# Optimization experiments

Measured on AMD Instinct MI355X. Metric: run time of the kernel, lower is better.

## Reference

```python
import jax, jax.numpy as jnp
import numpy as np

D_MODEL = 768
N_HEAD = 12
D_FF = 2048
KEEP_RATIO = 0.6
EPS = 1e-6


def rmsnorm(x, g):
    var = jnp.mean(x * x, axis=-1, keepdims=True)
    return x * jax.lax.rsqrt(var + EPS) * g


def setup_inputs() -> dict:
    key = jax.random.key(0)
    ks = jax.random.split(key, 16)
    B, S, D, F = 2, 2048, D_MODEL, D_FF
    s = 0.02
    inp = {
        "hidden": jax.random.normal(ks[0], (B, S, D), jnp.float32),
        "attn_mask": jnp.tril(jnp.ones((S, S), dtype=bool)),
        "temperature": 1,
        "wq": jax.random.normal(ks[1], (D, D), jnp.float32) * s,
        "wk": jax.random.normal(ks[2], (D, D), jnp.float32) * s,
        "wv": jax.random.normal(ks[3], (D, D), jnp.float32) * s,
        "wo": jax.random.normal(ks[4], (D, D), jnp.float32) * s,
        "w1": jax.random.normal(ks[5], (D, F), jnp.float32) * s,
        "w3": jax.random.normal(ks[6], (D, F), jnp.float32) * s,
        "w2": jax.random.normal(ks[7], (F, D), jnp.float32) * s,
        "g1": jnp.ones((D,), jnp.float32),
        "g2": jnp.ones((D,), jnp.float32),
        "w_mod": jax.random.normal(ks[8], (D,), jnp.float32) * s,
        "b_mod": jnp.zeros((), jnp.float32),
        "w_tok": jax.random.normal(ks[9], (D,), jnp.float32) * s,
        "b_tok": jnp.zeros((), jnp.float32),
        "w_gate": jax.random.normal(ks[10], (D, D), jnp.float32) * s,
        "b_gate": jnp.zeros((D,), jnp.float32),
    }
    return inp


def reference(hidden, attn_mask, temperature, wq, wk, wv, wo, w1, w3, w2,
              g1, g2, w_mod, b_mod, w_tok, b_tok, w_gate, b_gate):
    B, S, D = hidden.shape
    H = N_HEAD
    Dh = D // H

    # depth router: sigmoid(linear / temperature)
    depth_logits = jnp.einsum("bsd,d->bs", hidden, w_mod) + b_mod
    depth_probs = jax.nn.sigmoid(depth_logits / temperature)
    active = (depth_probs > 0.5).astype(hidden.dtype)[..., None]  # [B,S,1]

    normed = rmsnorm(hidden, g1)

    # token router: sigmoid scores, hard top-k keep mask at base keep ratio
    token_scores = jax.nn.sigmoid(jnp.einsum("bsd,d->bs", normed, w_tok) + b_tok)
    k = max(1, int(S * KEEP_RATIO))
    kth = jax.lax.top_k(token_scores, k)[0][:, -1:]  # [B,1]
    token_mask = (token_scores >= kth).astype(hidden.dtype)  # [B,S]

    # multi-head attention over normed
    q = jnp.einsum("bsd,de->bse", normed, wq).reshape(B, S, H, Dh)
    kk = jnp.einsum("bsd,de->bse", normed, wk).reshape(B, S, H, Dh)
    v = jnp.einsum("bsd,de->bse", normed, wv).reshape(B, S, H, Dh)
    logits = jnp.einsum("bqhd,bkhd->bhqk", q, kk) / jnp.sqrt(jnp.float32(Dh))
    logits = jnp.where(attn_mask[None, None, :, :], logits, jnp.float32(-1e9))
    probs = jax.nn.softmax(logits, axis=-1)
    ctx = jnp.einsum("bhqk,bkhd->bqhd", probs, v).reshape(B, S, D)
    attn_out = jnp.einsum("bsd,de->bse", ctx, wo)

    attn_out = attn_out * token_mask[..., None]
    hidden = hidden + attn_out * active  # dropout = identity (eval)

    # ACM gate: x * sigmoid(Wx + b)
    n2 = rmsnorm(hidden, g2)
    gated = n2 * jax.nn.sigmoid(jnp.einsum("bsd,de->bse", n2, w_gate) + b_gate)

    # SwiGLU MLP
    mlp = jnp.einsum("bsf,fd->bsd",
                     jax.nn.silu(jnp.einsum("bsd,df->bsf", gated, w1))
                     * jnp.einsum("bsd,df->bsf", gated, w3), w2)
    hidden = hidden + mlp * active
    return hidden, depth_probs, token_mask
```

## Files before the change

### kernel.cpp

```cpp
#include <hip/hip_runtime.h>


typedef float f32x4 __attribute__((ext_vector_type(4)));
typedef __bf16 bf16x8 __attribute__((ext_vector_type(8)));
typedef unsigned int u32;

#define DEV static __device__ __forceinline__

constexpr int SEQ = 2048, DIM = 768, NH = 12;
constexpr int KKEEP = 1228;

DEV f32x4 mfma16(bf16x8 a, bf16x8 b, f32x4 c) {
  return __builtin_amdgcn_mfma_f32_16x16x32_bf16(a, b, c, 0, 0, 0);
}
DEV float sigm(float x) { return 1.0f / (1.0f + __expf(-x)); }
DEV bf16x8 ld8(const __bf16* p) { return *reinterpret_cast<const bf16x8*>(p); }
DEV void st8(__bf16* p, bf16x8 v) { *reinterpret_cast<bf16x8*>(p) = v; }
DEV int swzo(int row, int u) { return row * 64 + ((u ^ (row & 7)) << 3); }

template <int NZ>
struct PtrPack { const float* s[NZ]; };

template <int NZ>
__global__ void k_transpose_castz(PtrPack<NZ> pp, __bf16* __restrict__ dst0,
                                  int K, int N, size_t dstride) {
  const float* __restrict__ src = pp.s[blockIdx.z];
  __bf16* __restrict__ dst = dst0 + (size_t)blockIdx.z * dstride;
  __shared__ float tile[32][33];
  const int tx = threadIdx.x, ty = threadIdx.y;
  const int n0 = blockIdx.x * 32, k0 = blockIdx.y * 32;
  for (int i = 0; i < 4; ++i)
    tile[ty + 8 * i][tx] = src[(size_t)(k0 + ty + 8 * i) * N + n0 + tx];
  __syncthreads();
  for (int i = 0; i < 4; ++i)
    dst[(size_t)(n0 + ty + 8 * i) * K + k0 + tx] = (__bf16)tile[tx][ty + 8 * i];
}

__global__ void k_transpose_bf(const __bf16* __restrict__ src,
                               __bf16* __restrict__ dst) {
  __shared__ __bf16 t64[64][66];
  const int tx = threadIdx.x, ty = threadIdx.y;
  const int c0 = blockIdx.x * 64, r0 = blockIdx.y * 64;
#pragma unroll
  for (int i = 0; i < 8; ++i) {
    union { u32 uu; __bf16 hh[2]; } cv;
    cv.uu = *reinterpret_cast<const u32*>(src + (size_t)(r0 + ty + 8 * i) * 768 +
                                          c0 + tx * 2);
    t64[ty + 8 * i][tx * 2] = cv.hh[0];
    t64[ty + 8 * i][tx * 2 + 1] = cv.hh[1];
  }
  __syncthreads();
#pragma unroll
  for (int i = 0; i < 8; ++i) {
    union { u32 uu; __bf16 hh[2]; } cv;
    cv.hh[0] = t64[tx * 2][ty + 8 * i];
    cv.hh[1] = t64[tx * 2 + 1][ty + 8 * i];
    *reinterpret_cast<u32*>(dst + (size_t)(c0 + ty + 8 * i) * 4096 + r0 + tx * 2) =
        cv.uu;
  }
}

__global__ __launch_bounds__(256) void k_router(
    const float* __restrict__ hid, const float* __restrict__ g1,
    const float* __restrict__ wmod, const float* __restrict__ bmod,
    const float* __restrict__ wtok, const float* __restrict__ btok,
    const int* __restrict__ temp, __bf16* __restrict__ normed,
    float* __restrict__ depth_out, float* __restrict__ actF,
    float* __restrict__ tokL) {
  const int t = blockIdx.x, tid = threadIdx.x;
  const float* x = hid + (size_t)t * DIM;
  float xs[3], gs[3], ss = 0.f, dm = 0.f, dt = 0.f;
  for (int j = 0; j < 3; ++j) {
    const int i = tid + 256 * j;
    const float xv = x[i], g = g1[i];
    xs[j] = xv; gs[j] = g;
    ss += xv * xv;
    dm += xv * wmod[i];
    dt += xv * g * wtok[i];
  }
  for (int m = 32; m >= 1; m >>= 1) {
    ss += __shfl_xor(ss, m);
    dm += __shfl_xor(dm, m);
    dt += __shfl_xor(dt, m);
  }
  __shared__ float red[4][3];
  if ((tid & 63) == 0) { red[tid >> 6][0] = ss; red[tid >> 6][1] = dm; red[tid >> 6][2] = dt; }
  __syncthreads();
  ss = red[0][0] + red[1][0] + red[2][0] + red[3][0];
  dm = red[0][1] + red[1][1] + red[2][1] + red[3][1];
  dt = red[0][2] + red[1][2] + red[2][2] + red[3][2];
  const float rms = rsqrtf(ss / 768.0f + 1e-6f);
  if (tid == 0) {
    const int iv = temp[0];
    const float T = (iv > -100000 && iv < 100000) ? (float)iv : __int_as_float(iv);
    const float z = (dm + bmod[0]) / T;
    depth_out[t] = sigm(z);
    actF[t] = z > 0.0f ? 1.0f : 0.0f;
    tokL[t] = rms * dt + btok[0];
  }
  for (int j = 0; j < 3; ++j) {
    const int i = tid + 256 * j;
    normed[(size_t)t * DIM + i] = (__bf16)(xs[j] * rms * gs[j]);
  }
}

__global__ __launch_bounds__(256) void k_count(
    const float* __restrict__ tokL, float* __restrict__ kth_out) {
  const int b = blockIdx.y, tid = threadIdx.x;
  __shared__ float vals[2048];
  const float* L = tokL + (size_t)b * 2048;
#pragma unroll
  for (int j = 0; j < 8; ++j) vals[tid + 256 * j] = L[tid + 256 * j];
  __syncthreads();
  const int cand = blockIdx.x * 128 + (tid >> 1);
  const int half = tid & 1;
  const float e = vals[cand];
  int gt = 0, ge = 0;
  const float4* v4 = reinterpret_cast<const float4*>(vals) + half * 256;
#pragma unroll 8
  for (int j = 0; j < 256; ++j) {
    const float4 q = v4[j];
    gt += (q.x > e) + (q.y > e) + (q.z > e) + (q.w > e);
    ge += (q.x >= e) + (q.y >= e) + (q.z >= e) + (q.w >= e);
  }
  gt += __shfl_xor(gt, 1);
  ge += __shfl_xor(ge, 1);
  if (half == 0 && gt < KKEEP && KKEEP <= ge) kth_out[b] = e;
}

__global__ __launch_bounds__(256) void k_mask(
    const float* __restrict__ tokL, const float* __restrict__ kth,
    const float* __restrict__ actF, float* __restrict__ mask_out,
    float* __restrict__ maskact) {
  const int i = blockIdx.x * 256 + threadIdx.x;
  const int b = i >> 11;
  const float m = (tokL[i] >= kth[b]) ? 1.f : 0.f;
  mask_out[i] = m;
  maskact[i] = m * actF[i];
}

__global__ __launch_bounds__(256) void k_rmsnorm2(
    const float* __restrict__ h2, const float* __restrict__ g2,
    __bf16* __restrict__ n2) {
  const int t = blockIdx.x, tid = threadIdx.x;
  const float* x = h2 + (size_t)t * DIM;
  float xs[3], ss = 0.f;
  for (int j = 0; j < 3; ++j) { const float v = x[tid + 256 * j]; xs[j] = v; ss += v * v; }
  for (int m = 32; m >= 1; m >>= 1) ss += __shfl_xor(ss, m);
  __shared__ float red[4];
  if ((tid & 63) == 0) red[tid >> 6] = ss;
  __syncthreads();
  ss = red[0] + red[1] + red[2] + red[3];
  const float rms = rsqrtf(ss / 768.0f + 1e-6f);
  for (int j = 0; j < 3; ++j) {
    const int i = tid + 256 * j;
    n2[(size_t)t * DIM + i] = (__bf16)(xs[j] * rms * g2[i]);
  }
}

template <int EPI, int MI>
__global__ __launch_bounds__(256) void k_gemm(
    const __bf16* __restrict__ A, const __bf16* __restrict__ BT,
    int N, int K, size_t bt_stride, size_t out_stride,
    __bf16* __restrict__ outB, float* __restrict__ outF,
    const float* __restrict__ epF, const __bf16* __restrict__ epB,
    const float* __restrict__ rowsc, const float* __restrict__ bias) {
  constexpr int BM = MI * 32;
  __shared__ __align__(16) __bf16 As[BM * 64];
  __shared__ __align__(16) __bf16 Bs[128 * 64];
  const int tid = threadIdx.x;
  const int lane = tid & 63, w = tid >> 6;
  const int wr = w >> 1, wc = w & 1;
  const int f = lane & 15, e = lane >> 4;
  const int m0 = blockIdx.y * BM, n0 = blockIdx.x * 128;
  const __bf16* Bz = BT + (size_t)blockIdx.z * bt_stride;

  const int rowA = (MI == 4) ? (tid >> 1) : (tid >> 2);
  const int uA0  = (MI == 4) ? ((tid & 1) * 4) : ((tid & 3) * 2);
  const int rowB = tid >> 1, uB0 = (tid & 1) * 4;
  const __bf16* ApR = A + (size_t)(m0 + rowA) * K;
  const __bf16* BpR = Bz + (size_t)(n0 + rowB) * K;

  bf16x8 ya[MI], yb[4];
  auto LOADY = [&](int k0) {
#pragma unroll
    for (int j = 0; j < MI; ++j) ya[j] = ld8(ApR + k0 + (uA0 + j) * 8);
#pragma unroll
    for (int j = 0; j < 4; ++j) yb[j] = ld8(BpR + k0 + (uB0 + j) * 8);
  };
  auto STORE = [&]() {
#pragma unroll
    for (int j = 0; j < MI; ++j) st8(&As[swzo(rowA, uA0 + j)], ya[j]);
#pragma unroll
    for (int j = 0; j < 4; ++j) st8(&Bs[swzo(rowB, uB0 + j)], yb[j]);
  };

  f32x4 acc[MI][4] = {};
  LOADY(0);
  for (int k0 = 0; k0 < K; k0 += 64) {
    __syncthreads();
    STORE();
    if (k0 + 64 < K) LOADY(k0 + 64);
    __syncthreads();
    bf16x8 afl[MI], afh[MI], bfl[4], bfh[4];
#pragma unroll
    for (int mi = 0; mi < MI; ++mi) {
      const int row = wr * (MI * 16) + mi * 16 + f;
      afl[mi] = ld8(&As[swzo(row, e)]);
      afh[mi] = ld8(&As[swzo(row, e + 4)]);
    }
#pragma unroll
    for (int ni = 0; ni < 4; ++ni) {
      const int row = wc * 64 + ni * 16 + f;
      bfl[ni] = ld8(&Bs[swzo(row, e)]);
      bfh[ni] = ld8(&Bs[swzo(row, e + 4)]);
    }
#pragma unroll
    for (int mi = 0; mi < MI; ++mi)
#pragma unroll
      for (int ni = 0; ni < 4; ++ni) {
        acc[mi][ni] = mfma16(afl[mi], bfl[ni], acc[mi][ni]);
        acc[mi][ni] = mfma16(afh[mi], bfh[ni], acc[mi][ni]);
      }
  }
  const size_t oz = (size_t)blockIdx.z * out_stride;
#pragma unroll
  for (int mi = 0; mi < MI; ++mi)
#pragma unroll
    for (int ni = 0; ni < 4; ++ni)
#pragma unroll
      for (int r2 = 0; r2 < 4; ++r2) {
        const int row = m0 + wr * (MI * 16) + mi * 16 + e * 4 + r2;
        const int col = n0 + wc * 64 + ni * 16 + f;
        const size_t idx = (size_t)row * N + col;
        const float c = acc[mi][ni][r2];
        if constexpr (EPI == 0) {
          outB[oz + idx] = (__bf16)c;
        } else if constexpr (EPI == 1) {
          outF[idx] = epF[idx] + c * rowsc[row];
        } else if constexpr (EPI == 2) {
          outB[idx] = (__bf16)((float)epB[idx] * sigm(c + bias[col]));
        } else {
          const float u = (float)epB[idx];
          outB[idx] = (__bf16)(u * sigm(u) * c);
        }
      }
}

__global__ __launch_bounds__(256) void k_attn(
    const __bf16* __restrict__ qb, const __bf16* __restrict__ kb,
    const __bf16* __restrict__ vT, __bf16* __restrict__ Opart,
    float* __restrict__ ml) {
  __shared__ __bf16 Ks[64 * 64];
  __shared__ __bf16 Vt[64 * 64];
  __shared__ __bf16 Pl[4][16][72];
  const int tid = threadIdx.x, lane = tid & 63, w = tid >> 6;
  const int f = lane & 15, e = lane >> 4;
  const int idx = 79 - (int)blockIdx.x;
  int g4, rel;
  if (idx < 8)       { g4 = 0; rel = idx; }
  else if (idx < 24) { g4 = 1; rel = idx - 8; }
  else if (idx < 48) { g4 = 2; rel = idx - 24; }
  else               { g4 = 3; rel = idx - 48; }
  const int qt = (g4 << 3) + rel / (g4 + 1);
  const int c  = rel % (g4 + 1);
  const int bh = blockIdx.y;
  const int b = bh / NH, h = bh % NH;
  const int slot = bh * 80 + idx;
  const int q0 = qt * 64;
  const int kt0 = c * 8;
  const int ntile = min(8, qt + 1 - kt0);
  const size_t base = (size_t)b * SEQ * DIM + (size_t)h * 64;
  const float SCALE2 = 0.125f * 1.4426950408889634f;

  const int qrow = q0 + w * 16 + f;
  const bf16x8 aq0 = ld8(qb + base + (size_t)qrow * DIM + e * 8);
  const bf16x8 aq1 = ld8(qb + base + (size_t)qrow * DIM + 32 + e * 8);
  float lsum[4] = {0.f, 0.f, 0.f, 0.f};
  f32x4 cacc[4];
  for (int g = 0; g < 4; ++g) cacc[g] = f32x4{0.f, 0.f, 0.f, 0.f};

  const int r1 = tid >> 2, u0 = tid & 3;
  const __bf16* kp = kb + base + (size_t)r1 * DIM;
  const __bf16* vp = vT + (size_t)(h * 64 + r1) * 4096 + b * 2048;

  bf16x8 rk0 = ld8(kp + (size_t)(kt0 * 64) * DIM + u0 * 8);
  bf16x8 rk1 = ld8(kp + (size_t)(kt0 * 64) * DIM + (u0 + 4) * 8);
  bf16x8 rv0 = ld8(vp + kt0 * 64 + u0 * 8);
  bf16x8 rv1 = ld8(vp + kt0 * 64 + (u0 + 4) * 8);

  for (int tt = 0; tt < ntile; ++tt) {
    const int kt = kt0 + tt;
    __syncthreads();
    st8(&Ks[swzo(r1, u0)], rk0);  st8(&Ks[swzo(r1, u0 + 4)], rk1);
    st8(&Vt[swzo(r1, u0)], rv0);  st8(&Vt[swzo(r1, u0 + 4)], rv1);
    if (tt + 1 < ntile) {
      const size_t ko = (size_t)((kt + 1) * 64) * DIM;
      rk0 = ld8(kp + ko + u0 * 8);  rk1 = ld8(kp + ko + (u0 + 4) * 8);
      const int vo = (kt + 1) * 64;
      rv0 = ld8(vp + vo + u0 * 8);  rv1 = ld8(vp + vo + (u0 + 4) * 8);
    }
    __syncthreads();

    f32x4 sacc[4];
#pragma unroll
    for (int g = 0; g < 4; ++g) {
      const int row = g * 16 + f;
      f32x4 z = f32x4{0.f, 0.f, 0.f, 0.f};
      z = mfma16(aq0, ld8(&Ks[swzo(row, e)]), z);
      z = mfma16(aq1, ld8(&Ks[swzo(row, e + 4)]), z);
      sacc[g] = z;
    }
    const bool need_mask = (kt == qt);
    const int qg = q0 + w * 16 + e * 4;
    float p[4][4];
#pragma unroll
    for (int g = 0; g < 4; ++g) {
      const int kg = kt * 64 + g * 16 + f;
#pragma unroll
      for (int r = 0; r < 4; ++r) {
        const float pv = (need_mask && (kg > qg + r))
                             ? 0.f
                             : exp2f(sacc[g][r] * SCALE2);
        p[g][r] = pv;
        lsum[r] += pv;
      }
    }
#pragma unroll
    for (int g = 0; g < 4; ++g)
#pragma unroll
      for (int r = 0; r < 4; ++r) Pl[w][e * 4 + r][g * 16 + f] = (__bf16)p[g][r];
    const bf16x8 ap0 = ld8(&Pl[w][f][e * 8]);
    const bf16x8 ap1 = ld8(&Pl[w][f][32 + e * 8]);
#pragma unroll
    for (int g = 0; g < 4; ++g) {
      const int row = g * 16 + f;
      cacc[g] = mfma16(ap0, ld8(&Vt[swzo(row, e)]), cacc[g]);
      cacc[g] = mfma16(ap1, ld8(&Vt[swzo(row, e + 4)]), cacc[g]);
    }
  }
  for (int m = 1; m < 16; m <<= 1)
#pragma unroll
    for (int r = 0; r < 4; ++r) lsum[r] += __shfl_xor(lsum[r], m);
  if (f == 0) {
#pragma unroll
    for (int r = 0; r < 4; ++r)
      ml[(size_t)slot * 64 + w * 16 + e * 4 + r] = lsum[r];
  }
#pragma unroll
  for (int g = 0; g < 4; ++g)
#pragma unroll
    for (int r = 0; r < 4; ++r) {
      const int row = w * 16 + e * 4 + r;
      Opart[(size_t)slot * 4096 + row * 64 + g * 16 + f] = (__bf16)cacc[g][r];
    }
}

__global__ __launch_bounds__(256) void k_attn_combine(
    const __bf16* __restrict__ Opart, const float* __restrict__ ml,
    __bf16* __restrict__ ctxb) {
  const int qt = blockIdx.x, bh = blockIdx.y;
  const int b = bh / NH, h = bh % NH;
  const int g = qt >> 3;
  const int sb = bh * 80 + 4 * g * (g + 1) + (qt & 7) * (g + 1);
  const int nch = g + 1;
  const int row = threadIdx.x >> 2, dh0 = (threadIdx.x & 3) * 16;

  float ltot = 0.f;
  float acc[16];
#pragma unroll
  for (int j = 0; j < 16; ++j) acc[j] = 0.f;
  for (int cc = 0; cc < nch; ++cc) {
    ltot += ml[(size_t)(sb + cc) * 64 + row];
    const __bf16* op = Opart + (size_t)(sb + cc) * 4096 + row * 64 + dh0;
    const bf16x8 o0 = ld8(op), o1 = ld8(op + 8);
#pragma unroll
    for (int j = 0; j < 8; ++j) {
      acc[j] += (float)o0[j];
      acc[8 + j] += (float)o1[j];
    }
  }
  const float rl = 1.0f / ltot;
  bf16x8 w0, w1;
#pragma unroll
  for (int j = 0; j < 8; ++j) {
    w0[j] = (__bf16)(acc[j] * rl);
    w1[j] = (__bf16)(acc[8 + j] * rl);
  }
  const size_t base = (size_t)b * SEQ * DIM + (size_t)h * 64;
  __bf16* dst = ctxb + base + (size_t)(qt * 64 + row) * DIM + dh0;
  st8(dst, w0);
  st8(dst + 8, w1);
}

extern "C" void kernel_launch(void* const* d_in, const int* in_sizes, int n_in,
                              void* d_out, int out_size, void* d_ws, size_t ws_size,
                              hipStream_t stream) {
  const float* hid   = (const float*)d_in[0];
  const int*   temp  = (const int*)d_in[2];
  const float* wq    = (const float*)d_in[3];
  const float* wk    = (const float*)d_in[4];
  const float* wv    = (const float*)d_in[5];
  const float* wo    = (const float*)d_in[6];
  const float* w1    = (const float*)d_in[7];
  const float* w3    = (const float*)d_in[8];
  const float* w2    = (const float*)d_in[9];
  const float* g1    = (const float*)d_in[10];
  const float* g2    = (const float*)d_in[11];
  const float* wmod  = (const float*)d_in[12];
  const float* bmod  = (const float*)d_in[13];
  const float* wtok  = (const float*)d_in[14];
  const float* btok  = (const float*)d_in[15];
  const float* wgate = (const float*)d_in[16];
  const float* bgate = (const float*)d_in[17];

  char* ws = (char*)d_ws;
  __bf16* WT = (__bf16*)ws;
  const size_t oWQ = 0, oWK = 589824, oWV = 1179648, oWO = 1769472,
               oWG = 2359296, oW1 = 2949120, oW3 = 4521984, oW2 = 6094848;
  __bf16* qbuf   = (__bf16*)(ws + 15335424);
  __bf16* kbuf   = qbuf + 3145728;
  __bf16* vbuf   = kbuf + 3145728;
  __bf16* Ubuf   = qbuf;
  __bf16* normed = (__bf16*)(ws + 34209792);
  __bf16* ctxb   = normed + 3145728;
  __bf16* n2buf  = ctxb + 3145728;
  __bf16* vTbuf  = normed;
  __bf16* tbuf   = normed;
  float*  h2     = (float*)(ws + 53084160);
  __bf16* gated  = (__bf16*)(ws + 65667072);
  __bf16* Opart  = (__bf16*)(ws + 53084160);
  float*  mlbuf  = (float*)(ws + 68812800);
  float*  tokL   = (float*)(ws + 71958528);
  float*  actF   = tokL + 4096;
  float*  maskact = actF + 4096;
  float*  kthbuf  = maskact + 4096;

  float* dout = (float*)d_out;
  float* out_hidden = dout;
  float* out_depth  = dout + 3145728;
  float* out_mask   = dout + 3145728 + 4096;

  const dim3 tb(32, 8);
  PtrPack<5> p5; p5.s[0]=wq; p5.s[1]=wk; p5.s[2]=wv; p5.s[3]=wo; p5.s[4]=wgate;
  k_transpose_castz<5><<<dim3(24, 24, 5), tb, 0, stream>>>(p5, WT + oWQ, 768, 768, 589824);
  PtrPack<2> p2; p2.s[0]=w1; p2.s[1]=w3;
  k_transpose_castz<2><<<dim3(64, 24, 2), tb, 0, stream>>>(p2, WT + oW1, 768, 2048, 1572864);
  PtrPack<1> p1; p1.s[0]=w2;
  k_transpose_castz<1><<<dim3(24, 64, 1), tb, 0, stream>>>(p1, WT + oW2, 2048, 768, 0);

  k_router<<<4096, 256, 0, stream>>>(hid, g1, wmod, bmod, wtok, btok, temp,
                                     normed, out_depth, actF, tokL);
  k_count<<<dim3(16, 2), 256, 0, stream>>>(tokL, kthbuf);
  k_mask<<<16, 256, 0, stream>>>(tokL, kthbuf, actF, out_mask, maskact);

  k_gemm<0, 4><<<dim3(6, 32, 3), 256, 0, stream>>>(
      normed, WT + oWQ, 768, 768, 589824, 3145728,
      qbuf, nullptr, nullptr, nullptr, nullptr, nullptr);

  k_transpose_bf<<<dim3(12, 64), tb, 0, stream>>>(vbuf, vTbuf);

  k_attn<<<dim3(80, 24), 256, 0, stream>>>(qbuf, kbuf, vTbuf, Opart, mlbuf);
  k_attn_combine<<<dim3(32, 24), 256, 0, stream>>>(Opart, mlbuf, ctxb);

  k_gemm<1, 2><<<dim3(6, 64, 1), 256, 0, stream>>>(
      ctxb, WT + oWO, 768, 768, 0, 0,
      nullptr, h2, hid, nullptr, maskact, nullptr);

  k_rmsnorm2<<<4096, 256, 0, stream>>>(h2, g2, n2buf);

  k_gemm<2, 2><<<dim3(6, 64, 1), 256, 0, stream>>>(
      n2buf, WT + oWG, 768, 768, 0, 0,
      gated, nullptr, nullptr, n2buf, nullptr, bgate);

  k_gemm<0, 4><<<dim3(16, 32, 1), 256, 0, stream>>>(
      gated, WT + oW1, 2048, 768, 0, 0,
      Ubuf, nullptr, nullptr, nullptr, nullptr, nullptr);

  k_gemm<3, 4><<<dim3(16, 32, 1), 256, 0, stream>>>(
      gated, WT + oW3, 2048, 768, 0, 0,
      tbuf, nullptr, nullptr, Ubuf, nullptr, nullptr);

  k_gemm<1, 2><<<dim3(6, 64, 1), 256, 0, stream>>>(
      tbuf, WT + oW2, 768, 2048, 0, 0,
      nullptr, out_hidden, h2, nullptr, actF, nullptr);

  (void)in_sizes; (void)n_in; (void)out_size; (void)ws_size;
}
```

Measured before the change: 214.8 us.

## Fuse V transpose into QKV GEMM epilogue and merge W1/W3 GEMMs

The QKV projection GEMM gains an epilogue that writes V directly in transposed layout as packed 4-element stores, which removes the separate transpose kernel. The two SwiGLU up-projection GEMMs are merged into one kernel that shares the A tile, keeps both accumulators and applies silu(u)*v in registers. This drops the intermediate U buffer round-trip through memory and one kernel launch. The cost is higher register and LDS use in the fused GEMM, which may lower occupancy, and strided transposed stores for V.

```diff
diff --git a/kernel.cpp b/kernel.cpp
--- a/kernel.cpp
+++ b/kernel.cpp
@@ -3,6 +3,7 @@
 
 typedef float f32x4 __attribute__((ext_vector_type(4)));
 typedef __bf16 bf16x8 __attribute__((ext_vector_type(8)));
+typedef __bf16 bf16x4 __attribute__((ext_vector_type(4)));
 typedef unsigned int u32;
 
 #define DEV static __device__ __forceinline__
@@ -34,30 +35,6 @@
   __syncthreads();
   for (int i = 0; i < 4; ++i)
     dst[(size_t)(n0 + ty + 8 * i) * K + k0 + tx] = (__bf16)tile[tx][ty + 8 * i];
-}
-
-__global__ void k_transpose_bf(const __bf16* __restrict__ src,
-                               __bf16* __restrict__ dst) {
-  __shared__ __bf16 t64[64][66];
-  const int tx = threadIdx.x, ty = threadIdx.y;
-  const int c0 = blockIdx.x * 64, r0 = blockIdx.y * 64;
-#pragma unroll
-  for (int i = 0; i < 8; ++i) {
-    union { u32 uu; __bf16 hh[2]; } cv;
-    cv.uu = *reinterpret_cast<const u32*>(src + (size_t)(r0 + ty + 8 * i) * 768 +
-                                          c0 + tx * 2);
-    t64[ty + 8 * i][tx * 2] = cv.hh[0];
-    t64[ty + 8 * i][tx * 2 + 1] = cv.hh[1];
-  }
-  __syncthreads();
-#pragma unroll
-  for (int i = 0; i < 8; ++i) {
-    union { u32 uu; __bf16 hh[2]; } cv;
-    cv.hh[0] = t64[tx * 2][ty + 8 * i];
-    cv.hh[1] = t64[tx * 2 + 1][ty + 8 * i];
-    *reinterpret_cast<u32*>(dst + (size_t)(c0 + ty + 8 * i) * 4096 + r0 + tx * 2) =
-        cv.uu;
-  }
 }
 
 __global__ __launch_bounds__(256) void k_router(
@@ -224,26 +201,134 @@
       }
   }
   const size_t oz = (size_t)blockIdx.z * out_stride;
-#pragma unroll
-  for (int mi = 0; mi < MI; ++mi)
+  if constexpr (EPI == 5) {
+    __bf16* vt = (__bf16*)outF;
+    const bool isv = (blockIdx.z == 2);
+#pragma unroll
+    for (int mi = 0; mi < MI; ++mi)
+#pragma unroll
+      for (int ni = 0; ni < 4; ++ni) {
+        const int row0 = m0 + wr * (MI * 16) + mi * 16 + e * 4;
+        const int col = n0 + wc * 64 + ni * 16 + f;
+        if (!isv) {
+#pragma unroll
+          for (int r2 = 0; r2 < 4; ++r2)
+            outB[oz + (size_t)(row0 + r2) * N + col] = (__bf16)acc[mi][ni][r2];
+        } else {
+          bf16x4 pk;
+#pragma unroll
+          for (int r2 = 0; r2 < 4; ++r2) pk[r2] = (__bf16)acc[mi][ni][r2];
+          *reinterpret_cast<bf16x4*>(&vt[(size_t)col * 4096 + row0]) = pk;
+        }
+      }
+  } else {
+#pragma unroll
+    for (int mi = 0; mi < MI; ++mi)
+#pragma unroll
+      for (int ni = 0; ni < 4; ++ni)
+#pragma unroll
+        for (int r2 = 0; r2 < 4; ++r2) {
+          const int row = m0 + wr * (MI * 16) + mi * 16 + e * 4 + r2;
+          const int col = n0 + wc * 64 + ni * 16 + f;
+          const size_t idx = (size_t)row * N + col;
+          const float c = acc[mi][ni][r2];
+          if constexpr (EPI == 0) {
+            outB[oz + idx] = (__bf16)c;
+          } else if constexpr (EPI == 1) {
+            outF[idx] = epF[idx] + c * rowsc[row];
+          } else if constexpr (EPI == 2) {
+            outB[idx] = (__bf16)((float)epB[idx] * sigm(c + bias[col]));
+          }
+        }
+  }
+}
+
+__global__ __launch_bounds__(256) void k_gemm13(
+    const __bf16* __restrict__ A, const __bf16* __restrict__ B1T,
+    const __bf16* __restrict__ B3T, __bf16* __restrict__ outT) {
+  __shared__ __align__(16) __bf16 As[64 * 64];
+  __shared__ __align__(16) __bf16 B1s[128 * 64];
+  __shared__ __align__(16) __bf16 B3s[128 * 64];
+  const int tid = threadIdx.x;
+  const int lane = tid & 63, w = tid >> 6;
+  const int wr = w >> 1, wc = w & 1;
+  const int f = lane & 15, e = lane >> 4;
+  const int m0 = blockIdx.y * 64, n0 = blockIdx.x * 128;
+  const int rowA = tid >> 2, uA0 = (tid & 3) * 2;
+  const int rowB = tid >> 1, uB0 = (tid & 1) * 4;
+  const __bf16* ApR = A + (size_t)(m0 + rowA) * 768;
+  const __bf16* B1R = B1T + (size_t)(n0 + rowB) * 768;
+  const __bf16* B3R = B3T + (size_t)(n0 + rowB) * 768;
+
+  bf16x8 ya[2], yb1[4], yb3[4];
+  auto LOADY = [&](int k0) {
+#pragma unroll
+    for (int j = 0; j < 2; ++j) ya[j] = ld8(ApR + k0 + (uA0 + j) * 8);
+#pragma unroll
+    for (int j = 0; j < 4; ++j) yb1[j] = ld8(B1R + k0 + (uB0 + j) * 8);
+#pragma unroll
+    for (int j = 0; j < 4; ++j) yb3[j] = ld8(B3R + k0 + (uB0 + j) * 8);
+  };
+  auto STORE = [&]() {
+#pragma unroll
+    for (int j = 0; j < 2; ++j) st8(&As[swzo(rowA, uA0 + j)], ya[j]);
+#pragma unroll
+    for (int j = 0; j < 4; ++j) st8(&B1s[swzo(rowB, uB0 + j)], yb1[j]);
+#pragma unroll
+    for (int j = 0; j < 4; ++j) st8(&B3s[swzo(rowB, uB0 + j)], yb3[j]);
+  };
+
+  f32x4 acc1[2][4] = {}, acc3[2][4] = {};
+  LOADY(0);
+  for (int k0 = 0; k0 < 768; k0 += 64) {
+    __syncthreads();
+    STORE();
+    if (k0 + 64 < 768) LOADY(k0 + 64);
+    __syncthreads();
+    bf16x8 afl[2], afh[2], bl[4], bh[4];
+#pragma unroll
+    for (int mi = 0; mi < 2; ++mi) {
+      const int row = wr * 32 + mi * 16 + f;
+      afl[mi] = ld8(&As[swzo(row, e)]);
+      afh[mi] = ld8(&As[swzo(row, e + 4)]);
+    }
+#pragma unroll
+    for (int ni = 0; ni < 4; ++ni) {
+      const int row = wc * 64 + ni * 16 + f;
+      bl[ni] = ld8(&B1s[swzo(row, e)]);
+      bh[ni] = ld8(&B1s[swzo(row, e + 4)]);
+    }
+#pragma unroll
+    for (int mi = 0; mi < 2; ++mi)
+#pragma unroll
+      for (int ni = 0; ni < 4; ++ni) {
+        acc1[mi][ni] = mfma16(afl[mi], bl[ni], acc1[mi][ni]);
+        acc1[mi][ni] = mfma16(afh[mi], bh[ni], acc1[mi][ni]);
+      }
+#pragma unroll
+    for (int ni = 0; ni < 4; ++ni) {
+      const int row = wc * 64 + ni * 16 + f;
+      bl[ni] = ld8(&B3s[swzo(row, e)]);
+      bh[ni] = ld8(&B3s[swzo(row, e + 4)]);
+    }
+#pragma unroll
+    for (int mi = 0; mi < 2; ++mi)
+#pragma unroll
+      for (int ni = 0; ni < 4; ++ni) {
+        acc3[mi][ni] = mfma16(afl[mi], bl[ni], acc3[mi][ni]);
+        acc3[mi][ni] = mfma16(afh[mi], bh[ni], acc3[mi][ni]);
+      }
+  }
+#pragma unroll
+  for (int mi = 0; mi < 2; ++mi)
 #pragma unroll
     for (int ni = 0; ni < 4; ++ni)
 #pragma unroll
       for (int r2 = 0; r2 < 4; ++r2) {
-        const int row = m0 + wr * (MI * 16) + mi * 16 + e * 4 + r2;
+        const int row = m0 + wr * 32 + mi * 16 + e * 4 + r2;
         const int col = n0 + wc * 64 + ni * 16 + f;
-        const size_t idx = (size_t)row * N + col;
-        const float c = acc[mi][ni][r2];
-        if constexpr (EPI == 0) {
-          outB[oz + idx] = (__bf16)c;
-        } else if constexpr (EPI == 1) {
-          outF[idx] = epF[idx] + c * rowsc[row];
-        } else if constexpr (EPI == 2) {
-          outB[idx] = (__bf16)((float)epB[idx] * sigm(c + bias[col]));
-        } else {
-          const float u = (float)epB[idx];
-          outB[idx] = (__bf16)(u * sigm(u) * c);
-        }
+        const float u = acc1[mi][ni][r2];
+        outT[(size_t)row * 2048 + col] = (__bf16)(u * sigm(u) * acc3[mi][ni][r2]);
       }
 }
 
@@ -420,12 +505,10 @@
                oWG = 2359296, oW1 = 2949120, oW3 = 4521984, oW2 = 6094848;
   __bf16* qbuf   = (__bf16*)(ws + 15335424);
   __bf16* kbuf   = qbuf + 3145728;
-  __bf16* vbuf   = kbuf + 3145728;
-  __bf16* Ubuf   = qbuf;
+  __bf16* vTbuf  = kbuf + 3145728;
   __bf16* normed = (__bf16*)(ws + 34209792);
   __bf16* ctxb   = normed + 3145728;
   __bf16* n2buf  = ctxb + 3145728;
-  __bf16* vTbuf  = normed;
   __bf16* tbuf   = normed;
   float*  h2     = (float*)(ws + 53084160);
   __bf16* gated  = (__bf16*)(ws + 65667072);
@@ -454,11 +537,9 @@
   k_count<<<dim3(16, 2), 256, 0, stream>>>(tokL, kthbuf);
   k_mask<<<16, 256, 0, stream>>>(tokL, kthbuf, actF, out_mask, maskact);
 
-  k_gemm<0, 4><<<dim3(6, 32, 3), 256, 0, stream>>>(
+  k_gemm<5, 4><<<dim3(6, 32, 3), 256, 0, stream>>>(
       normed, WT + oWQ, 768, 768, 589824, 3145728,
-      qbuf, nullptr, nullptr, nullptr, nullptr, nullptr);
-
-  k_transpose_bf<<<dim3(12, 64), tb, 0, stream>>>(vbuf, vTbuf);
+      qbuf, (float*)vTbuf, nullptr, nullptr, nullptr, nullptr);
 
   k_attn<<<dim3(80, 24), 256, 0, stream>>>(qbuf, kbuf, vTbuf, Opart, mlbuf);
   k_attn_combine<<<dim3(32, 24), 256, 0, stream>>>(Opart, mlbuf, ctxb);
@@ -473,13 +554,7 @@
       n2buf, WT + oWG, 768, 768, 0, 0,
       gated, nullptr, nullptr, n2buf, nullptr, bgate);
 
-  k_gemm<0, 4><<<dim3(16, 32, 1), 256, 0, stream>>>(
-      gated, WT + oW1, 2048, 768, 0, 0,
-      Ubuf, nullptr, nullptr, nullptr, nullptr, nullptr);
-
-  k_gemm<3, 4><<<dim3(16, 32, 1), 256, 0, stream>>>(
-      gated, WT + oW3, 2048, 768, 0, 0,
-      tbuf, nullptr, nullptr, Ubuf, nullptr, nullptr);
+  k_gemm13<<<dim3(16, 64), 256, 0, stream>>>(gated, WT + oW1, WT + oW3, tbuf);
 
   k_gemm<1, 2><<<dim3(6, 64, 1), 256, 0, stream>>>(
       tbuf, WT + oW2, 768, 2048, 0, 0,
```

Measured after the change: 205.2 us. 4.5% less time.
